# Kernel tuning notes

Hardware: AMD Instinct MI355X
Metric: run time of the kernel (lower is better)

## Reference

```python
import jax, jax.numpy as jnp
import numpy as np


def _gru_cell(x, h, W_ih, W_hh, b_ih, b_hh):
    # torch.nn.GRUCell semantics
    gi = x @ W_ih.T + b_ih          # [B, 3H]
    gh = h @ W_hh.T + b_hh          # [B, 3H]
    i_r, i_z, i_n = jnp.split(gi, 3, axis=-1)
    h_r, h_z, h_n = jnp.split(gh, 3, axis=-1)
    r = jax.nn.sigmoid(i_r + h_r)
    z = jax.nn.sigmoid(i_z + h_z)
    n = jnp.tanh(i_n + r * h_n)
    return (1.0 - z) * n + z * h


def setup_inputs() -> dict:
    B, H1, H2, WU, PL = 1024, 512, 512, 512, 512
    key = jax.random.key(0)
    ks = jax.random.split(key, 11)
    s1 = 1.0 / np.sqrt(H1)
    s2 = 1.0 / np.sqrt(H2)
    return {
        "input": jax.random.normal(ks[0], (B, WU + PL), dtype=jnp.float32),
        "W_ih1": jax.random.uniform(ks[1], (3 * H1, 1), jnp.float32, -s1, s1),
        "W_hh1": jax.random.uniform(ks[2], (3 * H1, H1), jnp.float32, -s1, s1),
        "b_ih1": jax.random.uniform(ks[3], (3 * H1,), jnp.float32, -s1, s1),
        "b_hh1": jax.random.uniform(ks[4], (3 * H1,), jnp.float32, -s1, s1),
        "W_ih2": jax.random.uniform(ks[5], (3 * H2, H1), jnp.float32, -s2, s2),
        "W_hh2": jax.random.uniform(ks[6], (3 * H2, H2), jnp.float32, -s2, s2),
        "b_ih2": jax.random.uniform(ks[7], (3 * H2,), jnp.float32, -s2, s2),
        "b_hh2": jax.random.uniform(ks[8], (3 * H2,), jnp.float32, -s2, s2),
        "W_lin": jax.random.uniform(ks[9], (1, H2), jnp.float32, -s2, s2),
        "b_lin": jax.random.uniform(ks[10], (1,), jnp.float32, -s2, s2),
        "warm_up_len": 512,
        "predict_len": 512,
    }


def reference(input, W_ih1, W_hh1, b_ih1, b_hh1, W_ih2, W_hh2, b_ih2, b_hh2,
              W_lin, b_lin, warm_up_len, predict_len):
    B = input.shape[0]
    H1 = W_hh1.shape[1]
    H2 = W_hh2.shape[1]

    def step(carry, x_t):
        h1, h2 = carry
        h1 = _gru_cell(x_t, h1, W_ih1, W_hh1, b_ih1, b_hh1)
        h2 = _gru_cell(h1, h2, W_ih2, W_hh2, b_ih2, b_hh2)
        out = h2 @ W_lin.T + b_lin   # [B, 1]
        return (h1, h2), out

    h1 = jnp.zeros((B, H1), dtype=input.dtype)
    h2 = jnp.zeros((B, H2), dtype=input.dtype)

    # warm-up (teacher-forced): initialize_sequence
    xs = jnp.swapaxes(input[:, :warm_up_len], 0, 1)[:, :, None]  # [WU, B, 1]
    (h1, h2), warm_outs = jax.lax.scan(step, (h1, h2), xs)       # warm_outs [WU, B, 1]

    def ar_step(carry, _):
        h1, h2, out = carry
        (h1, h2), new_out = step((h1, h2), out)
        return (h1, h2, new_out), new_out

    last_out = warm_outs[-1]
    _, ar_outs = jax.lax.scan(ar_step, (h1, h2, last_out), None, length=predict_len)

    all_outs = jnp.concatenate([warm_outs, ar_outs], axis=0)  # [WU+PL, B, 1]
    # torch.stack(outputs, 1).squeeze(2) -> [B, WU+PL]
    return jnp.swapaxes(all_outs[..., 0], 0, 1)
```

## Files before the change

### kernel.cpp

```cpp
#include <hip/hip_runtime.h>

#define NBLK 256
#define NTHR 512
#define HDIM 512
#define TSTEPS 1024
#define WUP 512
#define WPL 786432
#define HPL 524288
#define PAR 65536

typedef unsigned short u16;
typedef unsigned int u32;
typedef __bf16 bf16x8 __attribute__((ext_vector_type(8)));
typedef float f32x4 __attribute__((ext_vector_type(4)));
typedef int i32x4 __attribute__((ext_vector_type(4)));

typedef __attribute__((address_space(3))) void as3v;
typedef __attribute__((address_space(1))) const void as1cv;

__device__ __forceinline__ void gload16(const u16* g, char* l) {
  __builtin_amdgcn_global_load_lds((as1cv*)g, (as3v*)l, 16, 0, 0);
}
__device__ __forceinline__ i32x4 load_sc(const u16* p) {
  i32x4 r;
  asm volatile("global_load_dwordx4 %0, %1, off sc0 sc1" : "=v"(r) : "v"(p) : "memory");
  return r;
}

__device__ __forceinline__ u16 f2bf(float f) {
  u32 u = __float_as_uint(f);
  u += 0x7fffu + ((u >> 16) & 1u);
  return (u16)(u >> 16);
}
__device__ __forceinline__ float bf2f(u16 s) { return __uint_as_float(((u32)s) << 16); }
__device__ __forceinline__ float sigm(float v) { return 1.f / (1.f + __expf(-v)); }
__device__ __forceinline__ float tanh_(float v) {
  float e = __expf(2.f * v);
  return 1.f - 2.f / (e + 1.f);
}
__device__ __forceinline__ f32x4 MFMA(bf16x8 a, bf16x8 b, f32x4 c) {
  return __builtin_amdgcn_mfma_f32_16x16x32_bf16(a, b, c, 0, 0, 0);
}

__device__ __forceinline__ void g_arrive(int* gb) {
  __syncthreads();
  if (threadIdx.x == 0) {
    int old = __hip_atomic_fetch_add(gb, 1, __ATOMIC_RELEASE, __HIP_MEMORY_SCOPE_AGENT);
    if ((old & 15) == 15)
      __hip_atomic_fetch_add(gb + 32, 1, __ATOMIC_RELEASE, __HIP_MEMORY_SCOPE_AGENT);
  }
}
__device__ __forceinline__ void g_wait(int* gb, int target) {
  if (threadIdx.x == 0) {
    while (__hip_atomic_load(gb + 32, __ATOMIC_RELAXED, __HIP_MEMORY_SCOPE_AGENT) < target)
      __builtin_amdgcn_s_sleep(1);
  }
  __builtin_amdgcn_fence(__ATOMIC_ACQUIRE, "workgroup");
  __syncthreads();
}

__global__ __launch_bounds__(NTHR, 2) void gru_seq_kernel(
    const float* __restrict__ input, const float* __restrict__ Wih1,
    const float* __restrict__ Whh1, const float* __restrict__ bih1, const float* __restrict__ bhh1,
    const float* __restrict__ Wih2, const float* __restrict__ Whh2,
    const float* __restrict__ bih2, const float* __restrict__ bhh2,
    const float* __restrict__ Wlin, const float* __restrict__ blinp,
    float* __restrict__ dout, u16* __restrict__ wsp, float* __restrict__ outsc,
    int* __restrict__ bar) {
  __shared__ __align__(16) char smem[131072];
  const int wg = blockIdx.x, tid = threadIdx.x;
  const int lane = tid & 63, wv = tid >> 6;
  const int l15 = lane & 15, l4 = lane >> 4;
  const int rt = wv >> 1, ch = wv & 1;

  u16* Wh1h = wsp;           u16* Wh1l = wsp + WPL;
  u16* Wi2h = wsp + 2 * WPL; u16* Wi2l = wsp + 3 * WPL;
  u16* Wh2h = wsp + 4 * WPL; u16* Wh2l = wsp + 5 * WPL;
  u16* hb_  = wsp + 6 * WPL;
  u16* h1h = hb_;            u16* h1l = hb_ + 2 * HPL;
  u16* h2h = hb_ + 4 * HPL;  u16* h2l = hb_ + 6 * HPL;
  int* ibar = bar + 2048;

  for (int i = wg * NTHR + tid; i < 3 * WPL; i += NBLK * NTHR) {
    int m = i / WPL, r = i - m * WPL;
    const float* src = (m == 0) ? Whh1 : (m == 1) ? Wih2 : Whh2;
    u16* dh = (m == 0) ? Wh1h : (m == 1) ? Wi2h : Wh2h;
    u16* dl = (m == 0) ? Wh1l : (m == 1) ? Wi2l : Wh2l;
    float v = src[r];
    u16 hbv = f2bf(v);
    dh[r] = hbv; dl[r] = f2bf(v - bf2f(hbv));
  }
  __syncthreads();
  if (tid == 0) {
    int old = __hip_atomic_fetch_add(ibar, 1, __ATOMIC_RELEASE, __HIP_MEMORY_SCOPE_AGENT);
    if (old == NBLK - 1)
      __hip_atomic_fetch_add(ibar + 32, 1, __ATOMIC_RELEASE, __HIP_MEMORY_SCOPE_AGENT);
  }

  const int xm = wg >> 3;
  const int cb = (wg & 7) * 2 + (xm & 1);
  const int rb = xm >> 1;
  int* gb1 = bar + rb * 128;
  int* gb2 = bar + rb * 128 + 64;

  const int j = cb * 32 + ch * 16 + l15;
  const float blin = blinp[0];
  const float wi_r = Wih1[j], wi_z = Wih1[j + 512], wi_n = Wih1[j + 1024];
  const float bi_r = bih1[j], bi_z = bih1[j + 512], bi_n = bih1[j + 1024];
  const float bh_r = bhh1[j], bh_z = bhh1[j + 512], bh_n = bhh1[j + 1024];
  const float c2i_r = bih2[j], c2i_z = bih2[j + 512], c2i_n = bih2[j + 1024];
  const float c2h_r = bhh2[j], c2h_z = bhh2[j + 512], c2h_n = bhh2[j + 1024];
  const float wlj = Wlin[j];

  const u16* wptrA[6]; int wdstA[6];
#pragma unroll
  for (int i = 0; i < 6; ++i) {
    int off = 16384 + (wv * 6 + i) * 1024 + lane * 16;
    int loc = off - 16384;
    int lo = 0; if (loc >= 24576) { lo = 1; loc -= 24576; }
    int brow = loc >> 7, bir = loc & 127;
    int lb = bir ^ ((brow & 7) << 4);
    int mat = (brow >= 96) ? 1 : 0;
    int s = brow - 96 * mat;
    int g = s >> 5, r = s & 31;
    u32 eoff = (u32)(g * 512 + cb * 32 + r) * HDIM + (u32)(lb >> 1);
    wptrA[i] = (mat ? (lo ? Wh1l : Wh1h) : (lo ? Wi2l : Wi2h)) + eoff;
    wdstA[i] = 16384 + (wv * 6 + i) * 1024;
  }
  const u16* wptrH[3]; int wdstH[3];
#pragma unroll
  for (int i = 0; i < 3; ++i) {
    int off = 16384 + (wv * 3 + i) * 1024 + lane * 16;
    int loc = off - 16384;
    int lo = 0; if (loc >= 12288) { lo = 1; loc -= 12288; }
    int brow = loc >> 7, bir = loc & 127;
    int lb = bir ^ ((brow & 7) << 4);
    int g = brow >> 5, r = brow & 31;
    u32 eoff = (u32)(g * 512 + cb * 32 + r) * HDIM + (u32)(lb >> 1);
    wptrH[i] = (lo ? Wh2l : Wh2h) + eoff;
    wdstH[i] = 16384 + (wv * 3 + i) * 1024;
  }

  const int r_ = tid >> 3, kb_ = (tid & 7) * 16;
  const u32 rowel = (u32)(rb * 64 + r_) * HDIM + (u32)(kb_ >> 1);
  const u32 ldsAh = (u32)(r_ << 7) + (u32)(kb_ ^ ((r_ & 7) << 4));
  const u32 ldsAl = 8192 + ldsAh;

  const u32 swz = (u32)(l15 & 7) << 4;
  const u32 aoff = (u32)(16 * rt + l15) * 128;
  u32 boff[3];
#pragma unroll
  for (int g = 0; g < 3; ++g) boff[g] = (u32)(g * 32 + ch * 16 + l15) * 128;

  const f32x4 vzero = {0.f, 0.f, 0.f, 0.f};
  f32x4 acc1[3] = {vzero, vzero, vzero};
  float h1s[4] = {0.f, 0.f, 0.f, 0.f}, h2s[4] = {0.f, 0.f, 0.f, 0.f};

  if (tid == 0) {
    while (__hip_atomic_load(ibar + 32, __ATOMIC_RELAXED, __HIP_MEMORY_SCOPE_AGENT) < 1)
      __builtin_amdgcn_s_sleep(1);
  }
  __builtin_amdgcn_fence(__ATOMIC_ACQUIRE, "workgroup");
  __syncthreads();

#define GA_CHUNK(p) do { \
    const char* sm_ = smem + (p) * PAR; \
    _Pragma("unroll") \
    for (int kk = 0; kk < 2; ++kk) { \
      u32 kb = ((u32)(kk * 64) + (u32)(l4 * 16)) ^ swz; \
      bf16x8 ah = *(const bf16x8*)(sm_ + aoff + kb); \
      bf16x8 al = *(const bf16x8*)(sm_ + 8192 + aoff + kb); \
      _Pragma("unroll") \
      for (int g = 0; g < 3; ++g) { \
        bf16x8 bih = *(const bf16x8*)(sm_ + 16384 + boff[g] + kb); \
        bf16x8 buh = *(const bf16x8*)(sm_ + 28672 + boff[g] + kb); \
        bf16x8 bil = *(const bf16x8*)(sm_ + 40960 + boff[g] + kb); \
        bf16x8 bul = *(const bf16x8*)(sm_ + 53248 + boff[g] + kb); \
        acci[g] = MFMA(ah, bih, acci[g]); \
        acci[g] = MFMA(al, bih, acci[g]); \
        acci[g] = MFMA(ah, bil, acci[g]); \
        acn[g] = MFMA(ah, buh, acn[g]); \
        acn[g] = MFMA(al, buh, acn[g]); \
        acn[g] = MFMA(ah, bul, acn[g]); \
      } \
    } \
  } while (0)

#define GH_CHUNK(p) do { \
    const char* sm_ = smem + (p) * PAR; \
    _Pragma("unroll") \
    for (int kk = 0; kk < 2; ++kk) { \
      u32 kb = ((u32)(kk * 64) + (u32)(l4 * 16)) ^ swz; \
      bf16x8 ah = *(const bf16x8*)(sm_ + aoff + kb); \
      bf16x8 al = *(const bf16x8*)(sm_ + 8192 + aoff + kb); \
      _Pragma("unroll") \
      for (int g = 0; g < 3; ++g) { \
        bf16x8 bh = *(const bf16x8*)(sm_ + 16384 + boff[g] + kb); \
        bf16x8 bl = *(const bf16x8*)(sm_ + 28672 + boff[g] + kb); \
        acch[g] = MFMA(ah, bh, acch[g]); \
        acch[g] = MFMA(al, bh, acch[g]); \
        acch[g] = MFMA(ah, bl, acch[g]); \
      } \
    } \
  } while (0)

  for (int t = 0; t < TSTEPS; ++t) {
    const int cur = t & 1, prv = cur ^ 1;

    float xpre[4];
    if (t < WUP) {
#pragma unroll
      for (int rr = 0; rr < 4; ++rr)
        xpre[rr] = input[(rb * 64 + 16 * rt + l4 * 4 + rr) * 1024 + t];
    }

    if (t > 0) g_wait(gb2, t);

    if (cb == 0 && tid < 64) {
      int b = rb * 64 + tid;
      if (t > 0) {
        float osc = __hip_atomic_load(outsc + prv * 1024 + b, __ATOMIC_RELAXED,
                                      __HIP_MEMORY_SCOPE_AGENT);
        dout[b * 1024 + (t - 1)] = osc + blin;
      }
      outsc[cur * 1024 + b] = 0.f;
    }

    {
      u16* h1hc = h1h + cur * HPL;
      u16* h1lc = h1l + cur * HPL;
#pragma unroll
      for (int rr = 0; rr < 4; ++rr) {
        int b = rb * 64 + 16 * rt + l4 * 4 + rr;
        float x;
        if (t < WUP) {
          x = xpre[rr];
        } else {
          x = __hip_atomic_load(outsc + prv * 1024 + b, __ATOMIC_RELAXED,
                                __HIP_MEMORY_SCOPE_AGENT) + blin;
        }
        float r = sigm(fmaf(x, wi_r, bi_r) + acc1[0][rr] + bh_r);
        float z = sigm(fmaf(x, wi_z, bi_z) + acc1[1][rr] + bh_z);
        float n = tanh_(fmaf(r, acc1[2][rr] + bh_n, fmaf(x, wi_n, bi_n)));
        float h = (1.f - z) * n + z * h1s[rr];
        h1s[rr] = h;
        u16 hbv = f2bf(h);
        int idx = b * HDIM + j;
        h1hc[idx] = hbv; h1lc[idx] = f2bf(h - bf2f(hbv));
      }
    }
    g_arrive(gb1);

    f32x4 acch[3] = {vzero, vzero, vzero};
    if (t > 0) {
      const u16* pAh = h2h + prv * HPL + rowel;
      const u16* pAl = h2l + prv * HPL + rowel;
      i32x4 rh[2], rl[2];
      rh[0] = load_sc(pAh);
      rl[0] = load_sc(pAl);
#pragma unroll
      for (int i = 0; i < 3; ++i) gload16(wptrH[i], smem + wdstH[i]);
#pragma unroll
      for (int c = 0; c < 8; ++c) {
        char* bufc = smem + (c & 1) * PAR;
        asm volatile("s_waitcnt vmcnt(3)" ::: "memory");
        *(i32x4*)(bufc + ldsAh) = rh[c & 1];
        *(i32x4*)(bufc + ldsAl) = rl[c & 1];
        if (c < 7) {
          rh[(c + 1) & 1] = load_sc(pAh + (c + 1) * 64);
          rl[(c + 1) & 1] = load_sc(pAl + (c + 1) * 64);
          char* bufn = smem + ((c + 1) & 1) * PAR;
#pragma unroll
          for (int i = 0; i < 3; ++i) gload16(wptrH[i] + (c + 1) * 64, bufn + wdstH[i]);
          asm volatile("s_waitcnt vmcnt(5)" ::: "memory");
        } else {
          asm volatile("s_waitcnt vmcnt(0)" ::: "memory");
        }
        asm volatile("s_waitcnt lgkmcnt(0)" ::: "memory");
        __builtin_amdgcn_s_barrier();
        GH_CHUNK(c & 1);
        __builtin_amdgcn_s_barrier();
      }
    }
    g_wait(gb1, t + 1);

    f32x4 acci[3] = {vzero, vzero, vzero};
    f32x4 acn[3] = {vzero, vzero, vzero};
    {
      const u16* pAh = h1h + cur * HPL + rowel;
      const u16* pAl = h1l + cur * HPL + rowel;
      i32x4 rh[2], rl[2];
      rh[0] = load_sc(pAh);
      rl[0] = load_sc(pAl);
#pragma unroll
      for (int i = 0; i < 6; ++i) gload16(wptrA[i], smem + wdstA[i]);
#pragma unroll
      for (int c = 0; c < 8; ++c) {
        char* bufc = smem + (c & 1) * PAR;
        asm volatile("s_waitcnt vmcnt(6)" ::: "memory");
        *(i32x4*)(bufc + ldsAh) = rh[c & 1];
        *(i32x4*)(bufc + ldsAl) = rl[c & 1];
        if (c < 7) {
          rh[(c + 1) & 1] = load_sc(pAh + (c + 1) * 64);
          rl[(c + 1) & 1] = load_sc(pAl + (c + 1) * 64);
          char* bufn = smem + ((c + 1) & 1) * PAR;
#pragma unroll
          for (int i = 0; i < 6; ++i) gload16(wptrA[i] + (c + 1) * 64, bufn + wdstA[i]);
          asm volatile("s_waitcnt vmcnt(8)" ::: "memory");
        } else {
          asm volatile("s_waitcnt vmcnt(0)" ::: "memory");
        }
        asm volatile("s_waitcnt lgkmcnt(0)" ::: "memory");
        __builtin_amdgcn_s_barrier();
        GA_CHUNK(c & 1);
        __builtin_amdgcn_s_barrier();
      }
    }

    {
      u16* h2hc = h2h + cur * HPL;
      u16* h2lc = h2l + cur * HPL;
#pragma unroll
      for (int rr = 0; rr < 4; ++rr) {
        int b = rb * 64 + 16 * rt + l4 * 4 + rr;
        float r = sigm(acci[0][rr] + c2i_r + acch[0][rr] + c2h_r);
        float z = sigm(acci[1][rr] + c2i_z + acch[1][rr] + c2h_z);
        float n = tanh_(fmaf(r, acch[2][rr] + c2h_n, acci[2][rr] + c2i_n));
        float h = (1.f - z) * n + z * h2s[rr];
        h2s[rr] = h;
        u16 hbv = f2bf(h);
        int idx = b * HDIM + j;
        h2hc[idx] = hbv; h2lc[idx] = f2bf(h - bf2f(hbv));
        float v = h * wlj;
        v += __shfl_xor(v, 1);
        v += __shfl_xor(v, 2);
        v += __shfl_xor(v, 4);
        v += __shfl_xor(v, 8);
        if (l15 == 0) atomicAdd(outsc + cur * 1024 + b, v);
      }
    }
#pragma unroll
    for (int g = 0; g < 3; ++g) acc1[g] = acn[g];

    g_arrive(gb2);
  }

  g_wait(gb2, TSTEPS);
  if (cb == 0 && tid < 64) {
    int b = rb * 64 + tid;
    float osc = __hip_atomic_load(outsc + 1024 + b, __ATOMIC_RELAXED,
                                  __HIP_MEMORY_SCOPE_AGENT);
    dout[b * 1024 + 1023] = osc + blin;
  }
}

extern "C" void kernel_launch(void* const* d_in, const int* in_sizes, int n_in,
                              void* d_out, int out_size, void* d_ws, size_t ws_size,
                              hipStream_t stream) {
  (void)in_sizes; (void)n_in; (void)out_size; (void)ws_size;
  const float* input = (const float*)d_in[0];
  const float* Wih1  = (const float*)d_in[1];
  const float* Whh1  = (const float*)d_in[2];
  const float* bih1  = (const float*)d_in[3];
  const float* bhh1  = (const float*)d_in[4];
  const float* Wih2  = (const float*)d_in[5];
  const float* Whh2  = (const float*)d_in[6];
  const float* bih2  = (const float*)d_in[7];
  const float* bhh2  = (const float*)d_in[8];
  const float* Wlin  = (const float*)d_in[9];
  const float* blin  = (const float*)d_in[10];

  u16* wsp = (u16*)d_ws;
  size_t u16_count = (size_t)6 * WPL + (size_t)8 * HPL;
  float* outsc = (float*)((char*)d_ws + u16_count * 2);
  int* bar = (int*)((char*)outsc + 2048 * sizeof(float));

  hipMemsetAsync(bar, 0, 3 * 1024 * sizeof(int), stream);
  gru_seq_kernel<<<NBLK, NTHR, 0, stream>>>(input, Wih1, Whh1, bih1, bhh1,
                                            Wih2, Whh2, bih2, bhh2, Wlin, blin,
                                            (float*)d_out, wsp, outsc, bar);
}
```

Baseline: 43.34 ms.

## Preload all h-state chunks into registers and restructure chunk pipeline barriers

Loads all eight chunks of the previous h2 state (hi/lo bf16) into registers right after the grid barrier. The autoregressive feedback value is now read before the layer-1 update instead of inside it. The layer-2 input GEMM also issues all h1 loads up front. The per-chunk loop is changed so each iteration writes the next chunk to LDS and prefetches its weights before computing the current chunk, with one wait and barrier per chunk. The aim is to take global-load latency off the serialized per-chunk path, at the cost of more registers and full vmcnt(0) waits each chunk.

```diff
diff --git a/kernel.cpp b/kernel.cpp
--- a/kernel.cpp
+++ b/kernel.cpp
@@ -216,6 +216,25 @@
 
     if (t > 0) g_wait(gb2, t);
 
+    i32x4 rh2[8], rl2[8];
+    if (t > 0) {
+      const u16* pAh2 = h2h + prv * HPL + rowel;
+      const u16* pAl2 = h2l + prv * HPL + rowel;
+#pragma unroll
+      for (int c = 0; c < 8; ++c) {
+        rh2[c] = load_sc(pAh2 + c * 64);
+        rl2[c] = load_sc(pAl2 + c * 64);
+      }
+    }
+    if (t >= WUP) {
+#pragma unroll
+      for (int rr = 0; rr < 4; ++rr) {
+        int b = rb * 64 + 16 * rt + l4 * 4 + rr;
+        xpre[rr] = __hip_atomic_load(outsc + prv * 1024 + b, __ATOMIC_RELAXED,
+                                     __HIP_MEMORY_SCOPE_AGENT) + blin;
+      }
+    }
+
     if (cb == 0 && tid < 64) {
       int b = rb * 64 + tid;
       if (t > 0) {
@@ -232,13 +251,7 @@
 #pragma unroll
       for (int rr = 0; rr < 4; ++rr) {
         int b = rb * 64 + 16 * rt + l4 * 4 + rr;
-        float x;
-        if (t < WUP) {
-          x = xpre[rr];
-        } else {
-          x = __hip_atomic_load(outsc + prv * 1024 + b, __ATOMIC_RELAXED,
-                                __HIP_MEMORY_SCOPE_AGENT) + blin;
-        }
+        float x = xpre[rr];
         float r = sigm(fmaf(x, wi_r, bi_r) + acc1[0][rr] + bh_r);
         float z = sigm(fmaf(x, wi_z, bi_z) + acc1[1][rr] + bh_z);
         float n = tanh_(fmaf(r, acc1[2][rr] + bh_n, fmaf(x, wi_n, bi_n)));
@@ -253,32 +266,23 @@
 
     f32x4 acch[3] = {vzero, vzero, vzero};
     if (t > 0) {
-      const u16* pAh = h2h + prv * HPL + rowel;
-      const u16* pAl = h2l + prv * HPL + rowel;
-      i32x4 rh[2], rl[2];
-      rh[0] = load_sc(pAh);
-      rl[0] = load_sc(pAl);
+      *(i32x4*)(smem + ldsAh) = rh2[0];
+      *(i32x4*)(smem + ldsAl) = rl2[0];
 #pragma unroll
       for (int i = 0; i < 3; ++i) gload16(wptrH[i], smem + wdstH[i]);
+      asm volatile("s_waitcnt vmcnt(0) lgkmcnt(0)" ::: "memory");
+      __builtin_amdgcn_s_barrier();
 #pragma unroll
       for (int c = 0; c < 8; ++c) {
-        char* bufc = smem + (c & 1) * PAR;
-        asm volatile("s_waitcnt vmcnt(3)" ::: "memory");
-        *(i32x4*)(bufc + ldsAh) = rh[c & 1];
-        *(i32x4*)(bufc + ldsAl) = rl[c & 1];
         if (c < 7) {
-          rh[(c + 1) & 1] = load_sc(pAh + (c + 1) * 64);
-          rl[(c + 1) & 1] = load_sc(pAl + (c + 1) * 64);
           char* bufn = smem + ((c + 1) & 1) * PAR;
+          *(i32x4*)(bufn + ldsAh) = rh2[c + 1];
+          *(i32x4*)(bufn + ldsAl) = rl2[c + 1];
 #pragma unroll
           for (int i = 0; i < 3; ++i) gload16(wptrH[i] + (c + 1) * 64, bufn + wdstH[i]);
-          asm volatile("s_waitcnt vmcnt(5)" ::: "memory");
-        } else {
-          asm volatile("s_waitcnt vmcnt(0)" ::: "memory");
         }
-        asm volatile("s_waitcnt lgkmcnt(0)" ::: "memory");
-        __builtin_amdgcn_s_barrier();
         GH_CHUNK(c & 1);
+        asm volatile("s_waitcnt vmcnt(0) lgkmcnt(0)" ::: "memory");
         __builtin_amdgcn_s_barrier();
       }
     }
@@ -289,30 +293,30 @@
     {
       const u16* pAh = h1h + cur * HPL + rowel;
       const u16* pAl = h1l + cur * HPL + rowel;
-      i32x4 rh[2], rl[2];
-      rh[0] = load_sc(pAh);
-      rl[0] = load_sc(pAl);
 #pragma unroll
       for (int i = 0; i < 6; ++i) gload16(wptrA[i], smem + wdstA[i]);
+      i32x4 ra[8], rl_[8];
 #pragma unroll
       for (int c = 0; c < 8; ++c) {
-        char* bufc = smem + (c & 1) * PAR;
-        asm volatile("s_waitcnt vmcnt(6)" ::: "memory");
-        *(i32x4*)(bufc + ldsAh) = rh[c & 1];
-        *(i32x4*)(bufc + ldsAl) = rl[c & 1];
+        ra[c] = load_sc(pAh + c * 64);
+        rl_[c] = load_sc(pAl + c * 64);
+      }
+      asm volatile("s_waitcnt vmcnt(0)" ::: "memory");
+      *(i32x4*)(smem + ldsAh) = ra[0];
+      *(i32x4*)(smem + ldsAl) = rl_[0];
+      asm volatile("s_waitcnt lgkmcnt(0)" ::: "memory");
+      __builtin_amdgcn_s_barrier();
+#pragma unroll
+      for (int c = 0; c < 8; ++c) {
         if (c < 7) {
-          rh[(c + 1) & 1] = load_sc(pAh + (c + 1) * 64);
-          rl[(c + 1) & 1] = load_sc(pAl + (c + 1) * 64);
           char* bufn = smem + ((c + 1) & 1) * PAR;
+          *(i32x4*)(bufn + ldsAh) = ra[c + 1];
+          *(i32x4*)(bufn + ldsAl) = rl_[c + 1];
 #pragma unroll
           for (int i = 0; i < 6; ++i) gload16(wptrA[i] + (c + 1) * 64, bufn + wdstA[i]);
-          asm volatile("s_waitcnt vmcnt(8)" ::: "memory");
-        } else {
-          asm volatile("s_waitcnt vmcnt(0)" ::: "memory");
         }
-        asm volatile("s_waitcnt lgkmcnt(0)" ::: "memory");
-        __builtin_amdgcn_s_barrier();
         GA_CHUNK(c & 1);
+        asm volatile("s_waitcnt vmcnt(0) lgkmcnt(0)" ::: "memory");
         __builtin_amdgcn_s_barrier();
       }
     }
```

Result: slower. 56.17 ms (+29.6%).
